# Kernel tuning notes

Measured on AMD Instinct MI355X. Metric: run time of the kernel, lower is better.

Reference implementation:

```python
import jax, jax.numpy as jnp
import numpy as np

EPS = 0.001


def comp_interp_mat(grid):
    # grid: (N, H, W, 2) -> interp_mat: (N, HW, HW)
    N, H, W, _ = grid.shape
    HW = H * W
    g = grid.reshape(N, HW, 2)
    # position is valid only if in-range for ALL N grids (matches .all(0) in source)
    valid = ((g[..., 0] >= -EPS).all(0) & (g[..., 0] <= H - 1 + EPS).all(0)
             & (g[..., 1] >= -EPS).all(0) & (g[..., 1] <= W - 1 + EPS).all(0))  # (HW,)
    gx = jnp.clip(g[..., 0], EPS, H - 1 - EPS)
    gy = jnp.clip(g[..., 1], EPS, W - 1 - EPS)
    ix = jnp.floor(gx)
    iy = jnp.floor(gy)
    fx = gx - ix  # torch.frac == x - trunc(x); values are >0 here so same as x - floor(x)
    fy = gy - iy
    ix = ix.astype(jnp.int32)
    iy = iy.astype(jnp.int32)
    offs = jnp.array([[0, 0], [0, 1], [1, 0], [1, 1]], dtype=jnp.int32)
    # 4 distinct flattened corner indices per query position
    corners = (ix[..., None] + offs[:, 0]) * W + (iy[..., None] + offs[:, 1])  # (N, HW, 4)
    f0 = jnp.stack([1.0 - fx, fx], -1)  # (N, HW, 2)
    # NOTE: faithful to source, which does bmm(frac0, frac) with frac = (fx, fy),
    # i.e. NOT the standard (1-fy, fy) bilinear second factor.
    fr = jnp.stack([fx, fy], -1)  # (N, HW, 2)
    coeffs = (f0[..., :, None] * fr[..., None, :]).reshape(N, HW, 4)
    mat = jnp.zeros((N, HW, HW), grid.dtype)
    b = jnp.arange(N)[:, None, None]
    r = jnp.arange(HW)[None, :, None]
    mat = mat.at[b, r, corners].set(coeffs)  # 4 distinct cols per row -> set is safe
    # rows for invalid positions are zero (source only fills disk_mask rows)
    return mat * valid.astype(grid.dtype)[None, :, None]


def setup_inputs() -> dict:
    key = jax.random.key(0)
    k1, k2 = jax.random.split(key)
    N, C, H, W = 4, 128, 64, 64
    # uniform in [-1, H) so some positions fall outside the valid disk
    grid = jax.random.uniform(k1, (N, H, W, 2), jnp.float32, -1.0, float(H))
    x = jax.random.normal(k2, (N, C, H * W), jnp.float32)
    return {"x": x, "grid": grid}


def reference(x, grid):
    interp_mat = comp_interp_mat(grid)  # (N, HW, HW)
    # torch.bmm(x, interp_mat.transpose(1,2)) == einsum over shared j
    return jnp.einsum('ncj,nkj->nck', x, interp_mat)
```

## Files before the change

### kernel.cpp

```cpp
#include <hip/hip_runtime.h>

#define REF_EPS 0.001f

__global__ __launch_bounds__(256)
void precompute_kernel(const float* __restrict__ grid,
                       int4* __restrict__ corners_out,
                       float4* __restrict__ coeffs_out,
                       int N, int H, int W) {
    const int HW = H * W;
    const int k = blockIdx.x * 256 + threadIdx.x;
    if (k >= HW) return;

    const float2* gp = (const float2*)grid;
    const float hx = (float)(H - 1);
    const float wy = (float)(W - 1);

    int4   crn[8];
    float4 cf[8];
    bool valid = true;
    const int Nn = (N < 8) ? N : 8;

    for (int n = 0; n < Nn; ++n) {
        float2 g = gp[(size_t)n * HW + k];
        float g0 = g.x;
        float g1 = g.y;

        valid = valid && (g0 >= -REF_EPS) && (g0 <= hx + REF_EPS)
                      && (g1 >= -REF_EPS) && (g1 <= wy + REF_EPS);

        float gx = fminf(fmaxf(g0, REF_EPS), hx - REF_EPS);
        float gy = fminf(fmaxf(g1, REF_EPS), wy - REF_EPS);
        float ixf = floorf(gx);
        float iyf = floorf(gy);
        float fx = gx - ixf;
        float fy = gy - iyf;
        int ix = (int)ixf;
        int iy = (int)iyf;
        int c0 = ix * W + iy;
        crn[n] = make_int4(c0, c0 + 1, c0 + W, c0 + W + 1);
        float omfx = 1.0f - fx;
        cf[n] = make_float4(omfx * fx, omfx * fy, fx * fx, fx * fy);
    }

    const float vm = valid ? 1.0f : 0.0f;
    for (int n = 0; n < Nn; ++n) {
        size_t idx = (size_t)n * HW + k;
        corners_out[idx] = crn[n];
        float4 c = cf[n];
        coeffs_out[idx] = make_float4(c.x * vm, c.y * vm, c.z * vm, c.w * vm);
    }
}

__global__ __launch_bounds__(256)
void apply_kernel(const float* __restrict__ x,
                  const int4* __restrict__ corners,
                  const float4* __restrict__ coeffs,
                  float* __restrict__ out,
                  int C, int HW) {
    extern __shared__ float xs[];

    const int row = blockIdx.x;
    const int n = row / C;
    const int tid = threadIdx.x;

    const float* xrow = x + (size_t)row * HW;

    const float4* xv = (const float4*)xrow;
    const int nvec = HW >> 2;
    for (int i = tid; i < nvec; i += 256) {
        float4 v = xv[i];
        int b = i << 2;
        xs[b + 0] = v.x;
        xs[b + 1] = v.y;
        xs[b + 2] = v.z;
        xs[b + 3] = v.w;
    }
    for (int i = (nvec << 2) + tid; i < HW; i += 256) {
        xs[i] = xrow[i];
    }
    __syncthreads();

    const int4*   crow = corners + (size_t)n * HW;
    const float4* wrow = coeffs + (size_t)n * HW;
    float* orow = out + (size_t)row * HW;

    for (int k = tid; k < HW; k += 256) {
        int4 cr = crow[k];
        float4 w = wrow[k];
        float r = xs[cr.x] * w.x + xs[cr.y] * w.y
                + xs[cr.z] * w.z + xs[cr.w] * w.w;
        orow[k] = r;
    }
}

extern "C" void kernel_launch(void* const* d_in, const int* in_sizes, int n_in,
                              void* d_out, int out_size, void* d_ws, size_t ws_size,
                              hipStream_t stream) {
    const float* x    = (const float*)d_in[0];
    const float* grid = (const float*)d_in[1];
    float* out = (float*)d_out;

    const int H = 64, W = 64;
    const int HW = H * W;
    const int N = in_sizes[1] / (HW * 2);
    const int C = in_sizes[0] / (N * HW);

    int4*   corners = (int4*)d_ws;
    float4* coeffs  = (float4*)((char*)d_ws + (size_t)N * HW * sizeof(int4));

    const int blocksA = (HW + 255) / 256;
    hipLaunchKernelGGL(precompute_kernel, dim3(blocksA), dim3(256), 0, stream,
                       grid, corners, coeffs, N, H, W);

    const size_t shmem = (size_t)HW * sizeof(float);
    hipLaunchKernelGGL(apply_kernel, dim3(N * C), dim3(256), shmem, stream,
                       x, corners, coeffs, out, C, HW);
}
```

Measured before the change: 68.80 us.

## Fuse precompute into apply kernel, recomputing bilinear weights per row block

Removes the separate precompute kernel and its workspace round-trip. Each block now reads all N grids directly, computes validity and corner weights on the fly, and handles four outputs per thread with float4 stores and 1024-thread blocks. This saves a launch and the 32 bytes per position of corner and coefficient reads, but every one of the N*C blocks redoes the validity check across all N grids. That multiplies grid reads and ALU work per block.

```diff
diff --git a/kernel.cpp b/kernel.cpp
--- a/kernel.cpp
+++ b/kernel.cpp
@@ -2,94 +2,73 @@
 
 #define REF_EPS 0.001f
 
-__global__ __launch_bounds__(256)
-void precompute_kernel(const float* __restrict__ grid,
-                       int4* __restrict__ corners_out,
-                       float4* __restrict__ coeffs_out,
-                       int N, int H, int W) {
+__global__ __launch_bounds__(1024)
+void fused_remap_kernel(const float* __restrict__ x,
+                        const float* __restrict__ grid,
+                        float* __restrict__ out,
+                        int N, int C, int H, int W) {
     const int HW = H * W;
-    const int k = blockIdx.x * 256 + threadIdx.x;
-    if (k >= HW) return;
-
-    const float2* gp = (const float2*)grid;
-    const float hx = (float)(H - 1);
-    const float wy = (float)(W - 1);
-
-    int4   crn[8];
-    float4 cf[8];
-    bool valid = true;
-    const int Nn = (N < 8) ? N : 8;
-
-    for (int n = 0; n < Nn; ++n) {
-        float2 g = gp[(size_t)n * HW + k];
-        float g0 = g.x;
-        float g1 = g.y;
-
-        valid = valid && (g0 >= -REF_EPS) && (g0 <= hx + REF_EPS)
-                      && (g1 >= -REF_EPS) && (g1 <= wy + REF_EPS);
-
-        float gx = fminf(fmaxf(g0, REF_EPS), hx - REF_EPS);
-        float gy = fminf(fmaxf(g1, REF_EPS), wy - REF_EPS);
-        float ixf = floorf(gx);
-        float iyf = floorf(gy);
-        float fx = gx - ixf;
-        float fy = gy - iyf;
-        int ix = (int)ixf;
-        int iy = (int)iyf;
-        int c0 = ix * W + iy;
-        crn[n] = make_int4(c0, c0 + 1, c0 + W, c0 + W + 1);
-        float omfx = 1.0f - fx;
-        cf[n] = make_float4(omfx * fx, omfx * fy, fx * fx, fx * fy);
-    }
-
-    const float vm = valid ? 1.0f : 0.0f;
-    for (int n = 0; n < Nn; ++n) {
-        size_t idx = (size_t)n * HW + k;
-        corners_out[idx] = crn[n];
-        float4 c = cf[n];
-        coeffs_out[idx] = make_float4(c.x * vm, c.y * vm, c.z * vm, c.w * vm);
-    }
-}
-
-__global__ __launch_bounds__(256)
-void apply_kernel(const float* __restrict__ x,
-                  const int4* __restrict__ corners,
-                  const float4* __restrict__ coeffs,
-                  float* __restrict__ out,
-                  int C, int HW) {
     extern __shared__ float xs[];
 
     const int row = blockIdx.x;
     const int n = row / C;
     const int tid = threadIdx.x;
 
-    const float* xrow = x + (size_t)row * HW;
-
-    const float4* xv = (const float4*)xrow;
+    const float4* xv = (const float4*)(x + (size_t)row * HW);
+    float4* xsv = (float4*)xs;
     const int nvec = HW >> 2;
-    for (int i = tid; i < nvec; i += 256) {
-        float4 v = xv[i];
-        int b = i << 2;
-        xs[b + 0] = v.x;
-        xs[b + 1] = v.y;
-        xs[b + 2] = v.z;
-        xs[b + 3] = v.w;
-    }
-    for (int i = (nvec << 2) + tid; i < HW; i += 256) {
-        xs[i] = xrow[i];
+    for (int i = tid; i < nvec; i += 1024) {
+        xsv[i] = xv[i];
     }
     __syncthreads();
 
-    const int4*   crow = corners + (size_t)n * HW;
-    const float4* wrow = coeffs + (size_t)n * HW;
-    float* orow = out + (size_t)row * HW;
+    const float hx = (float)(H - 1);
+    const float wy = (float)(W - 1);
+    const float4* g4 = (const float4*)grid;
+    float4* ov = (float4*)(out + (size_t)row * HW);
 
-    for (int k = tid; k < HW; k += 256) {
-        int4 cr = crow[k];
-        float4 w = wrow[k];
-        float r = xs[cr.x] * w.x + xs[cr.y] * w.y
-                + xs[cr.z] * w.z + xs[cr.w] * w.w;
-        orow[k] = r;
+    for (int k0 = tid << 2; k0 < HW; k0 += 1024 << 2) {
+        bool valid[4] = {true, true, true, true};
+        float g0n[4], g1n[4];
+        for (int m = 0; m < N; ++m) {
+            size_t base = ((size_t)m * HW + k0) >> 1;
+            float4 a = g4[base];
+            float4 b = g4[base + 1];
+            valid[0] = valid[0] && (a.x >= -REF_EPS) && (a.x <= hx + REF_EPS)
+                                && (a.y >= -REF_EPS) && (a.y <= wy + REF_EPS);
+            valid[1] = valid[1] && (a.z >= -REF_EPS) && (a.z <= hx + REF_EPS)
+                                && (a.w >= -REF_EPS) && (a.w <= wy + REF_EPS);
+            valid[2] = valid[2] && (b.x >= -REF_EPS) && (b.x <= hx + REF_EPS)
+                                && (b.y >= -REF_EPS) && (b.y <= wy + REF_EPS);
+            valid[3] = valid[3] && (b.z >= -REF_EPS) && (b.z <= hx + REF_EPS)
+                                && (b.w >= -REF_EPS) && (b.w <= wy + REF_EPS);
+            if (m == n) {
+                g0n[0] = a.x; g1n[0] = a.y;
+                g0n[1] = a.z; g1n[1] = a.w;
+                g0n[2] = b.x; g1n[2] = b.y;
+                g0n[3] = b.z; g1n[3] = b.w;
+            }
+        }
+
+        float4 res;
+        float* resp = &res.x;
+        #pragma unroll
+        for (int j = 0; j < 4; ++j) {
+            float gx = fminf(fmaxf(g0n[j], REF_EPS), hx - REF_EPS);
+            float gy = fminf(fmaxf(g1n[j], REF_EPS), wy - REF_EPS);
+            float ixf = floorf(gx);
+            float iyf = floorf(gy);
+            float fx = gx - ixf;
+            float fy = gy - iyf;
+            int c0 = (int)ixf * W + (int)iyf;
+            float omfx = 1.0f - fx;
+            float r = xs[c0]         * (omfx * fx)
+                    + xs[c0 + 1]     * (omfx * fy)
+                    + xs[c0 + W]     * (fx * fx)
+                    + xs[c0 + W + 1] * (fx * fy);
+            resp[j] = valid[j] ? r : 0.0f;
+        }
+        ov[k0 >> 2] = res;
     }
 }
 
@@ -105,14 +84,7 @@
     const int N = in_sizes[1] / (HW * 2);
     const int C = in_sizes[0] / (N * HW);
 
-    int4*   corners = (int4*)d_ws;
-    float4* coeffs  = (float4*)((char*)d_ws + (size_t)N * HW * sizeof(int4));
-
-    const int blocksA = (HW + 255) / 256;
-    hipLaunchKernelGGL(precompute_kernel, dim3(blocksA), dim3(256), 0, stream,
-                       grid, corners, coeffs, N, H, W);
-
     const size_t shmem = (size_t)HW * sizeof(float);
-    hipLaunchKernelGGL(apply_kernel, dim3(N * C), dim3(256), shmem, stream,
-                       x, corners, coeffs, out, C, HW);
+    hipLaunchKernelGGL(fused_remap_kernel, dim3(N * C), dim3(1024), shmem, stream,
+                       x, grid, out, N, C, H, W);
 }
```

New measurement: 65.93 us. 4.2% less time.
